# Performance work log

Hardware: AMD Instinct MI355X
Metric: run time of the kernel (lower is better)

The kernel has to match this reference:

```python
import jax, jax.numpy as jnp
import numpy as np

N_NODES = 50000
N_EDGES = 800000
NODE_DIM = 64
EDGE_DIM = 16
HIDDEN = 128
EPS = 1e-5


def _linear_init(key, fan_in, fan_out):
    k1, k2 = jax.random.split(key)
    bound = 1.0 / np.sqrt(fan_in)
    W = jax.random.uniform(k1, (fan_in, fan_out), minval=-bound, maxval=bound, dtype=jnp.float32)
    b = jax.random.uniform(k2, (fan_out,), minval=-bound, maxval=bound, dtype=jnp.float32)
    return W, b


def batchnorm(h, gamma, beta):
    # BatchNorm1d in training mode: batch mean/var (biased), eps=1e-5
    mu = jnp.mean(h, axis=0, keepdims=True)
    var = jnp.mean((h - mu) ** 2, axis=0, keepdims=True)
    return (h - mu) * jax.lax.rsqrt(var + EPS) * gamma + beta


def setup_inputs() -> dict:
    key = jax.random.key(0)
    ks = jax.random.split(key, 8)
    x = jax.random.normal(ks[0], (N_NODES, NODE_DIM), dtype=jnp.float32)
    edge_index = jax.random.randint(ks[1], (2, N_EDGES), 0, N_NODES, dtype=jnp.int64)
    edge_attr = jax.random.normal(ks[2], (N_EDGES, EDGE_DIM), dtype=jnp.float32)
    We1, be1 = _linear_init(ks[3], 2 * NODE_DIM + EDGE_DIM, HIDDEN)
    We2, be2 = _linear_init(ks[4], HIDDEN, HIDDEN)
    Wm, bm = _linear_init(ks[5], HIDDEN, HIDDEN)
    Wn1, bn1 = _linear_init(ks[6], NODE_DIM + HIDDEN, HIDDEN)
    Wn2, bn2 = _linear_init(ks[7], HIDDEN, HIDDEN)
    ones = jnp.ones((HIDDEN,), jnp.float32)
    zeros = jnp.zeros((HIDDEN,), jnp.float32)
    return dict(x=x, edge_index=edge_index, edge_attr=edge_attr,
                We1=We1, be1=be1, ge=ones, bbe=zeros, We2=We2, be2=be2,
                Wm=Wm, bm=bm,
                Wn1=Wn1, bn1=bn1, gn=ones, bbn=zeros, Wn2=Wn2, bn2=bn2)


def reference(x, edge_index, edge_attr, We1, be1, ge, bbe, We2, be2, Wm, bm, Wn1, bn1, gn, bbn, Wn2, bn2):
    row, col = edge_index[0], edge_index[1]
    # gather + concat -> edge network (Linear, BN, ReLU, Linear)
    edge_input = jnp.concatenate([x[row], x[col], edge_attr], axis=-1)  # [E, 2n+e]
    h = jax.nn.relu(batchnorm(edge_input @ We1 + be1, ge, bbe))
    edge_features = h @ We2 + be2
    # message MLP (Linear, ReLU)
    messages = jax.nn.relu(edge_features @ Wm + bm)  # [E, H]
    # scatter-add into source nodes
    agg = jax.ops.segment_sum(messages, row, num_segments=N_NODES)  # [N, H]
    # node network (Linear, BN, ReLU, Linear)
    node_input = jnp.concatenate([x, agg], axis=-1)
    hn = jax.nn.relu(batchnorm(node_input @ Wn1 + bn1, gn, bbn))
    return hn @ Wn2 + bn2
```

## Files before the change

### kernel.cpp

```cpp
#include <hip/hip_runtime.h>
#include <stdint.h>

#define NNODES 50000
#define NEDGES 800000
#define H 128
#define BN_EPS 1e-5f

typedef short short8 __attribute__((ext_vector_type(8)));
typedef float f32x4 __attribute__((ext_vector_type(4)));

__device__ __forceinline__ float bf2f(unsigned short u) {
    unsigned int v = ((unsigned int)u) << 16;
    return __uint_as_float(v);
}
__device__ __forceinline__ unsigned short f2bf(float f) {
    unsigned int x = __float_as_uint(f);
    return (unsigned short)((x + 0x7FFFu + ((x >> 16) & 1u)) >> 16);
}
__device__ __forceinline__ short8 s8z() { short8 z = {0,0,0,0,0,0,0,0}; return z; }

template<int KB>
__device__ __forceinline__ void gemm_tile(const short* __restrict__ sA, const int SK,
                                          const unsigned short* __restrict__ WT, const int RK,
                                          const int n0, f32x4 acc[4][4], const int lane) {
    const int mr = lane & 15, quad = lane >> 4;
    const short* W = (const short*)WT;
    #pragma unroll
    for (int kb = 0; kb < KB; ++kb) {
        short8 a[4];
        #pragma unroll
        for (int mt = 0; mt < 4; ++mt)
            a[mt] = *(const short8*)&sA[(mt*16 + mr)*SK + kb*32 + quad*8];
        #pragma unroll
        for (int nt = 0; nt < 4; ++nt) {
            short8 b = *(const short8*)&W[(size_t)(n0 + nt*16 + mr)*RK + kb*32 + quad*8];
            #pragma unroll
            for (int mt = 0; mt < 4; ++mt)
                acc[mt][nt] = __builtin_amdgcn_mfma_f32_16x16x32_bf16(a[mt], b, acc[mt][nt], 0, 0, 0);
        }
    }
}

__global__ void k_fold(const float* __restrict__ We2, const float* __restrict__ be2,
                       const float* __restrict__ Wm, const float* __restrict__ bm,
                       float* __restrict__ W2m, float* __restrict__ b2m) {
    int j = threadIdx.x;
    int i = blockIdx.x;
    if (i < H) {
        float acc = 0.f;
        for (int k = 0; k < H; ++k) acc = fmaf(We2[i*H + k], Wm[k*H + j], acc);
        W2m[i*H + j] = acc;
    } else {
        float acc = bm[j];
        for (int k = 0; k < H; ++k) acc = fmaf(be2[k], Wm[k*H + j], acc);
        b2m[j] = acc;
    }
}

__global__ void k_prep2(const float* __restrict__ We1, const float* __restrict__ Wn1,
                        const float* __restrict__ Wn2, const float* __restrict__ W2m,
                        unsigned short* __restrict__ WabT, unsigned short* __restrict__ Wn1T,
                        unsigned short* __restrict__ Wn2T, unsigned short* __restrict__ W2mT) {
    int i = blockIdx.x*256 + threadIdx.x;
    if (i < 16384) {
        int n = i >> 6, k = i & 63;
        WabT[n*64 + k] = f2bf(We1[(n < 128 ? k : 64 + k)*H + (n & 127)]);
    } else if (i < 40960) {
        int j = i - 16384; int n = j / 192, k = j - n*192;
        Wn1T[n*192 + k] = f2bf(Wn1[k*H + n]);
    } else if (i < 57344) {
        int j = i - 40960; int n = j >> 7, k = j & 127;
        Wn2T[n*H + k] = f2bf(Wn2[k*H + n]);
    } else if (i < 73728) {
        int j = i - 57344; int n = j >> 7, k = j & 127;
        W2mT[n*H + k] = f2bf(W2m[k*H + n]);
    }
}

__global__ void k_count(const int* __restrict__ ei, int* __restrict__ cnt) {
    int e = blockIdx.x*256 + threadIdx.x;
    if (e < NEDGES) atomicAdd(&cnt[ei[e]], 1);
}

__global__ void k_scan(const int* __restrict__ cnt, int* __restrict__ offsets,
                       int* __restrict__ cursor) {
    __shared__ int wsum[16];
    __shared__ int carry;
    const int tid = threadIdx.x;
    const int lane = tid & 63, wid = tid >> 6;
    if (tid == 0) carry = 0;
    for (int base = 0; base < NNODES; base += 1024) {
        int i = base + tid;
        int v = (i < NNODES) ? cnt[i] : 0;
        int xv = v;
        #pragma unroll
        for (int off = 1; off < 64; off <<= 1) {
            int y = __shfl_up(xv, off);
            if (lane >= off) xv += y;
        }
        if (lane == 63) wsum[wid] = xv;
        __syncthreads();
        if (tid == 0) {
            int a = carry;
            #pragma unroll
            for (int j = 0; j < 16; ++j) { int t = wsum[j]; wsum[j] = a; a += t; }
            carry = a;
        }
        __syncthreads();
        int excl = wsum[wid] + xv - v;
        if (i < NNODES) { offsets[i] = excl; cursor[i] = excl; }
        __syncthreads();
    }
    if (tid == 0) offsets[NNODES] = carry;
}

__global__ void k_scatter(const int* __restrict__ ei, int* __restrict__ cursor,
                          int* __restrict__ elist) {
    int e = blockIdx.x*256 + threadIdx.x;
    if (e < NEDGES) {
        int p = atomicAdd(&cursor[ei[e]], 1);
        elist[p] = e;
    }
}

__launch_bounds__(256)
__global__ void k_T(const float* __restrict__ x, const unsigned short* __restrict__ WabT,
                    unsigned short* __restrict__ T) {
    __shared__ short sA[128*72];
    const int tid = threadIdx.x;
    const int n0b = blockIdx.x*128;
    {
        const int rowl = tid >> 1, half = (tid & 1)*32;
        const int node = n0b + rowl;
        const bool ok = node < NNODES;
        #pragma unroll
        for (int c = 0; c < 4; ++c) {
            int k0 = half + c*8;
            short8 o = s8z();
            if (ok) {
                float4 a = *(const float4*)&x[node*64 + k0];
                float4 b = *(const float4*)&x[node*64 + k0 + 4];
                o[0]=(short)f2bf(a.x); o[1]=(short)f2bf(a.y); o[2]=(short)f2bf(a.z); o[3]=(short)f2bf(a.w);
                o[4]=(short)f2bf(b.x); o[5]=(short)f2bf(b.y); o[6]=(short)f2bf(b.z); o[7]=(short)f2bf(b.w);
            }
            *(short8*)&sA[rowl*72 + k0] = o;
        }
    }
    __syncthreads();
    const int wave = tid >> 6, lane = tid & 63;
    const int m0 = (wave & 1)*64;
    const int n0 = blockIdx.y*128 + (wave >> 1)*64;
    f32x4 acc[4][4];
    f32x4 z = {0.f, 0.f, 0.f, 0.f};
    #pragma unroll
    for (int mt = 0; mt < 4; ++mt)
        #pragma unroll
        for (int nt = 0; nt < 4; ++nt) acc[mt][nt] = z;
    gemm_tile<2>(sA + m0*72, 72, WabT, 64, n0, acc, lane);
    const int mr = lane & 15, quad = lane >> 4;
    #pragma unroll
    for (int nt = 0; nt < 4; ++nt) {
        int j = n0 + nt*16 + mr;
        #pragma unroll
        for (int mt = 0; mt < 4; ++mt) {
            int nb = n0b + m0 + mt*16 + quad*4;
            #pragma unroll
            for (int r = 0; r < 4; ++r) {
                int node = nb + r;
                if (node < NNODES) T[(size_t)node*256 + j] = f2bf(acc[mt][nt][r]);
            }
        }
    }
}

__launch_bounds__(256)
__global__ void k_gather(const unsigned short* __restrict__ T, const int* __restrict__ ei,
                         const float* __restrict__ ea, const float* __restrict__ We1,
                         const float* __restrict__ be1, unsigned short* __restrict__ h1,
                         float* __restrict__ gS, float* __restrict__ gSS) {
    __shared__ float sS[H], sSS[H];
    const int tid = threadIdx.x;
    if (tid < H) { sS[tid] = 0.f; sSS[tid] = 0.f; }
    const int li = tid & 15;
    const int slot = (blockIdx.x*256 + tid) >> 4;
    float4 wcA[16], wcB[16];
    #pragma unroll
    for (int k = 0; k < 16; ++k) {
        wcA[k] = *(const float4*)&We1[(128 + k)*H + li*8];
        wcB[k] = *(const float4*)&We1[(128 + k)*H + li*8 + 4];
    }
    float be[8];
    #pragma unroll
    for (int i = 0; i < 8; ++i) be[i] = be1[li*8 + i];
    float s[8], ss[8];
    #pragma unroll
    for (int i = 0; i < 8; ++i) { s[i] = 0.f; ss[i] = 0.f; }
    for (int it = 0; it < 40; ++it) {
        int e = slot + it*20000;
        int row = ei[e], col = ei[NEDGES + e];
        short8 t1 = *(const short8*)&T[(size_t)row*256 + li*8];
        short8 t2 = *(const short8*)&T[(size_t)col*256 + 128 + li*8];
        float v[8];
        #pragma unroll
        for (int i = 0; i < 8; ++i)
            v[i] = bf2f((unsigned short)t1[i]) + bf2f((unsigned short)t2[i]) + be[i];
        #pragma unroll
        for (int k = 0; k < 16; ++k) {
            float a = ea[e*16 + k];
            v[0] = fmaf(a, wcA[k].x, v[0]); v[1] = fmaf(a, wcA[k].y, v[1]);
            v[2] = fmaf(a, wcA[k].z, v[2]); v[3] = fmaf(a, wcA[k].w, v[3]);
            v[4] = fmaf(a, wcB[k].x, v[4]); v[5] = fmaf(a, wcB[k].y, v[5]);
            v[6] = fmaf(a, wcB[k].z, v[6]); v[7] = fmaf(a, wcB[k].w, v[7]);
        }
        short8 o;
        #pragma unroll
        for (int i = 0; i < 8; ++i) {
            o[i] = (short)f2bf(v[i]);
            s[i] += v[i]; ss[i] += v[i]*v[i];
        }
        *(short8*)&h1[(size_t)e*H + li*8] = o;
    }
    __syncthreads();
    #pragma unroll
    for (int i = 0; i < 8; ++i) {
        atomicAdd(&sS[li*8 + i], s[i]);
        atomicAdd(&sSS[li*8 + i], ss[i]);
    }
    __syncthreads();
    if (tid < H) { atomicAdd(&gS[tid], sS[tid]); atomicAdd(&gSS[tid], sSS[tid]); }
}

__global__ void k_stats(const float* __restrict__ S, const float* __restrict__ SS,
                        const float* __restrict__ g, const float* __restrict__ b,
                        float invCount, float* __restrict__ scale, float* __restrict__ shift) {
    int j = threadIdx.x;
    float mu = S[j]*invCount;
    float var = SS[j]*invCount - mu*mu;
    float sc = rsqrtf(var + BN_EPS)*g[j];
    scale[j] = sc;
    shift[j] = b[j] - mu*sc;
}

__launch_bounds__(256)
__global__ void k_edge2(unsigned short* __restrict__ hb,
                        const float* __restrict__ scale, const float* __restrict__ shift,
                        const unsigned short* __restrict__ W2mT, const float* __restrict__ b2m) {
    __shared__ short sA[128*136];
    const int tid = threadIdx.x;
    const size_t e0 = (size_t)blockIdx.x*128;
    {
        const int rowl = tid >> 1, half = (tid & 1)*64;
        const size_t base = (e0 + rowl)*H + half;
        #pragma unroll
        for (int c = 0; c < 8; ++c) {
            int k0 = half + c*8;
            short8 raw = *(const short8*)&hb[base + c*8];
            float4 sc0 = *(const float4*)&scale[k0], sc1 = *(const float4*)&scale[k0 + 4];
            float4 sh0 = *(const float4*)&shift[k0], sh1 = *(const float4*)&shift[k0 + 4];
            short8 o;
            o[0] = (short)f2bf(fmaxf(fmaf(bf2f((unsigned short)raw[0]), sc0.x, sh0.x), 0.f));
            o[1] = (short)f2bf(fmaxf(fmaf(bf2f((unsigned short)raw[1]), sc0.y, sh0.y), 0.f));
            o[2] = (short)f2bf(fmaxf(fmaf(bf2f((unsigned short)raw[2]), sc0.z, sh0.z), 0.f));
            o[3] = (short)f2bf(fmaxf(fmaf(bf2f((unsigned short)raw[3]), sc0.w, sh0.w), 0.f));
            o[4] = (short)f2bf(fmaxf(fmaf(bf2f((unsigned short)raw[4]), sc1.x, sh1.x), 0.f));
            o[5] = (short)f2bf(fmaxf(fmaf(bf2f((unsigned short)raw[5]), sc1.y, sh1.y), 0.f));
            o[6] = (short)f2bf(fmaxf(fmaf(bf2f((unsigned short)raw[6]), sc1.z, sh1.z), 0.f));
            o[7] = (short)f2bf(fmaxf(fmaf(bf2f((unsigned short)raw[7]), sc1.w, sh1.w), 0.f));
            *(short8*)&sA[rowl*136 + k0] = o;
        }
    }
    __syncthreads();
    const int wave = tid >> 6, lane = tid & 63;
    const int m0 = (wave & 1)*64, n0 = (wave >> 1)*64;
    f32x4 acc[4][4];
    f32x4 z = {0.f, 0.f, 0.f, 0.f};
    #pragma unroll
    for (int mt = 0; mt < 4; ++mt)
        #pragma unroll
        for (int nt = 0; nt < 4; ++nt) acc[mt][nt] = z;
    gemm_tile<4>(sA + m0*136, 136, W2mT, 128, n0, acc, lane);
    const int mr = lane & 15, quad = lane >> 4;
    #pragma unroll
    for (int nt = 0; nt < 4; ++nt) {
        int j = n0 + nt*16 + mr;
        float bias = b2m[j];
        #pragma unroll
        for (int mt = 0; mt < 4; ++mt) {
            size_t eb = e0 + m0 + mt*16 + quad*4;
            #pragma unroll
            for (int r = 0; r < 4; ++r)
                hb[(eb + r)*H + j] = f2bf(fmaxf(acc[mt][nt][r] + bias, 0.f));
        }
    }
}

__launch_bounds__(256)
__global__ void k_agg(const unsigned short* __restrict__ msg, const int* __restrict__ offsets,
                      const int* __restrict__ elist, unsigned short* __restrict__ aggb) {
    const int n = blockIdx.x*4 + (threadIdx.x >> 6);
    const int lane = threadIdx.x & 63;
    const int s0 = offsets[n], t0 = offsets[n + 1];
    float a0 = 0.f, a1 = 0.f;
    for (int i = s0; i < t0; ++i) {
        int e = elist[i];
        unsigned int u = *(const unsigned int*)&msg[(size_t)e*H + lane*2];
        a0 += bf2f((unsigned short)(u & 0xFFFFu));
        a1 += bf2f((unsigned short)(u >> 16));
    }
    unsigned int o = (unsigned int)f2bf(a0) | ((unsigned int)f2bf(a1) << 16);
    *(unsigned int*)&aggb[(size_t)n*H + lane*2] = o;
}

__launch_bounds__(256)
__global__ void k_node1(const float* __restrict__ x, const unsigned short* __restrict__ aggb,
                        const unsigned short* __restrict__ Wn1T, const float* __restrict__ bn1,
                        float* __restrict__ h2, float* __restrict__ gS, float* __restrict__ gSS) {
    __shared__ short sA[128*200];
    __shared__ float sS[H], sSS[H];
    const int tid = threadIdx.x;
    if (tid < H) { sS[tid] = 0.f; sSS[tid] = 0.f; }
    const int n0b = blockIdx.x*128;
    {
        const int rowl = tid >> 1, half = (tid & 1)*96;
        const int node = n0b + rowl;
        const bool ok = node < NNODES;
        #pragma unroll
        for (int c = 0; c < 12; ++c) {
            int k0 = half + c*8;
            short8 o = s8z();
            if (ok) {
                if (k0 < 64) {
                    float4 a = *(const float4*)&x[node*64 + k0];
                    float4 b = *(const float4*)&x[node*64 + k0 + 4];
                    o[0]=(short)f2bf(a.x); o[1]=(short)f2bf(a.y); o[2]=(short)f2bf(a.z); o[3]=(short)f2bf(a.w);
                    o[4]=(short)f2bf(b.x); o[5]=(short)f2bf(b.y); o[6]=(short)f2bf(b.z); o[7]=(short)f2bf(b.w);
                } else {
                    o = *(const short8*)&aggb[(size_t)node*H + (k0 - 64)];
                }
            }
            *(short8*)&sA[rowl*200 + k0] = o;
        }
    }
    __syncthreads();
    const int wave = tid >> 6, lane = tid & 63;
    const int m0 = (wave & 1)*64, n0 = (wave >> 1)*64;
    f32x4 acc[4][4];
    f32x4 z = {0.f, 0.f, 0.f, 0.f};
    #pragma unroll
    for (int mt = 0; mt < 4; ++mt)
        #pragma unroll
        for (int nt = 0; nt < 4; ++nt) acc[mt][nt] = z;
    gemm_tile<6>(sA + m0*200, 200, Wn1T, 192, n0, acc, lane);
    const int mr = lane & 15, quad = lane >> 4;
    #pragma unroll
    for (int nt = 0; nt < 4; ++nt) {
        int j = n0 + nt*16 + mr;
        float bias = bn1[j];
        float s = 0.f, ssum = 0.f;
        #pragma unroll
        for (int mt = 0; mt < 4; ++mt) {
            int nb = n0b + m0 + mt*16 + quad*4;
            #pragma unroll
            for (int r = 0; r < 4; ++r) {
                int node = nb + r;
                if (node < NNODES) {
                    float v = acc[mt][nt][r] + bias;
                    h2[(size_t)node*H + j] = v;
                    s += v; ssum += v*v;
                }
            }
        }
        atomicAdd(&sS[j], s);
        atomicAdd(&sSS[j], ssum);
    }
    __syncthreads();
    if (tid < H) { atomicAdd(&gS[tid], sS[tid]); atomicAdd(&gSS[tid], sSS[tid]); }
}

__launch_bounds__(256)
__global__ void k_node2(const float* __restrict__ h2, const float* __restrict__ scale,
                        const float* __restrict__ shift, const unsigned short* __restrict__ Wn2T,
                        const float* __restrict__ bn2, float* __restrict__ out) {
    __shared__ short sA[128*136];
    const int tid = threadIdx.x;
    const int n0b = blockIdx.x*128;
    {
        const int rowl = tid >> 1, half = (tid & 1)*64;
        const int node = n0b + rowl;
        const bool ok = node < NNODES;
        #pragma unroll
        for (int c = 0; c < 8; ++c) {
            int k0 = half + c*8;
            short8 o = s8z();
            if (ok) {
                float4 a = *(const float4*)&h2[(size_t)node*H + k0];
                float4 b = *(const float4*)&h2[(size_t)node*H + k0 + 4];
                float4 sc0 = *(const float4*)&scale[k0], sc1 = *(const float4*)&scale[k0 + 4];
                float4 sh0 = *(const float4*)&shift[k0], sh1 = *(const float4*)&shift[k0 + 4];
                o[0] = (short)f2bf(fmaxf(fmaf(a.x, sc0.x, sh0.x), 0.f));
                o[1] = (short)f2bf(fmaxf(fmaf(a.y, sc0.y, sh0.y), 0.f));
                o[2] = (short)f2bf(fmaxf(fmaf(a.z, sc0.z, sh0.z), 0.f));
                o[3] = (short)f2bf(fmaxf(fmaf(a.w, sc0.w, sh0.w), 0.f));
                o[4] = (short)f2bf(fmaxf(fmaf(b.x, sc1.x, sh1.x), 0.f));
                o[5] = (short)f2bf(fmaxf(fmaf(b.y, sc1.y, sh1.y), 0.f));
                o[6] = (short)f2bf(fmaxf(fmaf(b.z, sc1.z, sh1.z), 0.f));
                o[7] = (short)f2bf(fmaxf(fmaf(b.w, sc1.w, sh1.w), 0.f));
            }
            *(short8*)&sA[rowl*136 + k0] = o;
        }
    }
    __syncthreads();
    const int wave = tid >> 6, lane = tid & 63;
    const int m0 = (wave & 1)*64, n0 = (wave >> 1)*64;
    f32x4 acc[4][4];
    f32x4 z = {0.f, 0.f, 0.f, 0.f};
    #pragma unroll
    for (int mt = 0; mt < 4; ++mt)
        #pragma unroll
        for (int nt = 0; nt < 4; ++nt) acc[mt][nt] = z;
    gemm_tile<4>(sA + m0*136, 136, Wn2T, 128, n0, acc, lane);
    const int mr = lane & 15, quad = lane >> 4;
    #pragma unroll
    for (int nt = 0; nt < 4; ++nt) {
        int j = n0 + nt*16 + mr;
        float bias = bn2[j];
        #pragma unroll
        for (int mt = 0; mt < 4; ++mt) {
            int nb = n0b + m0 + mt*16 + quad*4;
            #pragma unroll
            for (int r = 0; r < 4; ++r) {
                int node = nb + r;
                if (node < NNODES) out[(size_t)node*H + j] = acc[mt][nt][r] + bias;
            }
        }
    }
}

extern "C" void kernel_launch(void* const* d_in, const int* in_sizes, int n_in,
                              void* d_out, int out_size, void* d_ws, size_t ws_size,
                              hipStream_t stream) {
    (void)in_sizes; (void)n_in; (void)out_size; (void)ws_size;
    const float* x   = (const float*)d_in[0];
    const int*   ei  = (const int*)d_in[1];
    const float* ea  = (const float*)d_in[2];
    const float* We1 = (const float*)d_in[3];
    const float* be1 = (const float*)d_in[4];
    const float* ge  = (const float*)d_in[5];
    const float* bbe = (const float*)d_in[6];
    const float* We2 = (const float*)d_in[7];
    const float* be2 = (const float*)d_in[8];
    const float* Wm  = (const float*)d_in[9];
    const float* bm  = (const float*)d_in[10];
    const float* Wn1 = (const float*)d_in[11];
    const float* bn1 = (const float*)d_in[12];
    const float* gn  = (const float*)d_in[13];
    const float* bbn = (const float*)d_in[14];
    const float* Wn2 = (const float*)d_in[15];
    const float* bn2 = (const float*)d_in[16];
    float* out = (float*)d_out;

    char* ws = (char*)d_ws;
    unsigned short* hb   = (unsigned short*)(ws);
    unsigned short* aggb = (unsigned short*)(ws + 204800000);
    unsigned short* Tbuf = (unsigned short*)(ws + 217600000);
    float*          h2   = (float*)(ws + 217600000);
    int* cnt     = (int*)(ws + 243200000);
    int* offsets = (int*)(ws + 243400000);
    int* cursor  = (int*)(ws + 243600064);
    int* elist   = (int*)(ws + 243800064);
    float* S1     = (float*)(ws + 247000064);
    float* SS1    = S1 + 128;
    float* S2     = S1 + 256;
    float* SS2    = S1 + 384;
    float* scale1 = S1 + 512;
    float* shift1 = S1 + 640;
    float* scale2 = S1 + 768;
    float* shift2 = S1 + 896;
    float* W2m = (float*)(ws + 247004160);
    float* b2m = (float*)(ws + 247069696);
    unsigned short* WabT = (unsigned short*)(ws + 247070208);
    unsigned short* Wn1T = (unsigned short*)(ws + 247102976);
    unsigned short* Wn2T = (unsigned short*)(ws + 247152128);
    unsigned short* W2mT = (unsigned short*)(ws + 247184896);

    hipMemsetAsync(cnt, 0, NNODES*sizeof(int), stream);
    hipMemsetAsync(S1, 0, 512*sizeof(float), stream);

    k_fold<<<H + 1, H, 0, stream>>>(We2, be2, Wm, bm, W2m, b2m);
    k_prep2<<<288, 256, 0, stream>>>(We1, Wn1, Wn2, W2m, WabT, Wn1T, Wn2T, W2mT);
    k_count<<<NEDGES/256, 256, 0, stream>>>(ei, cnt);
    k_scan<<<1, 1024, 0, stream>>>(cnt, offsets, cursor);
    k_scatter<<<NEDGES/256, 256, 0, stream>>>(ei, cursor, elist);
    k_T<<<dim3(391, 2), 256, 0, stream>>>(x, WabT, Tbuf);
    k_gather<<<1250, 256, 0, stream>>>(Tbuf, ei, ea, We1, be1, hb, S1, SS1);
    k_stats<<<1, H, 0, stream>>>(S1, SS1, ge, bbe, 1.0f/NEDGES, scale1, shift1);
    k_edge2<<<NEDGES/128, 256, 0, stream>>>(hb, scale1, shift1, W2mT, b2m);
    k_agg<<<NNODES/4, 256, 0, stream>>>(hb, offsets, elist, aggb);
    k_node1<<<391, 256, 0, stream>>>(x, aggb, Wn1T, bn1, h2, S2, SS2);
    k_stats<<<1, H, 0, stream>>>(S2, SS2, gn, bbn, 1.0f/NNODES, scale2, shift2);
    k_node2<<<391, 256, 0, stream>>>(h2, scale2, shift2, Wn2T, bn2, out);
}
```

Measured before the change: 751.0 us.

## Recompute edge pre-activations in fused edge kernel and segment-reduce messages in-block

The gather kernel now only accumulates BatchNorm statistics and no longer writes the 800k x 128 bf16 pre-activation buffer. A new fused kernel walks edges in CSR (sorted by source) order, recomputes the pre-activation from the projected node table and edge attributes, applies BN and ReLU, runs the folded MLP GEMM, and reduces messages per source node in shared memory. Each run is written directly to an fp32 aggregate buffer, or atomically added when the run spans block boundaries. This removes the large intermediate write and read and the separate aggregation kernel, at the cost of computing the first layer twice, a serial per-column segment scan, and a memset of the aggregate buffer.

```diff
diff --git a/kernel.cpp b/kernel.cpp
--- a/kernel.cpp
+++ b/kernel.cpp
@@ -174,10 +174,10 @@
 }
 
 __launch_bounds__(256)
-__global__ void k_gather(const unsigned short* __restrict__ T, const int* __restrict__ ei,
-                         const float* __restrict__ ea, const float* __restrict__ We1,
-                         const float* __restrict__ be1, unsigned short* __restrict__ h1,
-                         float* __restrict__ gS, float* __restrict__ gSS) {
+__global__ void k_stats_edges(const unsigned short* __restrict__ T, const int* __restrict__ ei,
+                              const float* __restrict__ ea, const float* __restrict__ We1,
+                              const float* __restrict__ be1,
+                              float* __restrict__ gS, float* __restrict__ gSS) {
     __shared__ float sS[H], sSS[H];
     const int tid = threadIdx.x;
     if (tid < H) { sS[tid] = 0.f; sSS[tid] = 0.f; }
@@ -195,30 +195,34 @@
     float s[8], ss[8];
     #pragma unroll
     for (int i = 0; i < 8; ++i) { s[i] = 0.f; ss[i] = 0.f; }
-    for (int it = 0; it < 40; ++it) {
-        int e = slot + it*20000;
+    const float4* ea4 = (const float4*)ea;
+    for (int it = 0; it < 20; ++it) {
+        int e = slot + it*40000;
         int row = ei[e], col = ei[NEDGES + e];
         short8 t1 = *(const short8*)&T[(size_t)row*256 + li*8];
         short8 t2 = *(const short8*)&T[(size_t)col*256 + 128 + li*8];
+        float4 ev[4];
+        #pragma unroll
+        for (int q = 0; q < 4; ++q) ev[q] = ea4[e*4 + q];
         float v[8];
         #pragma unroll
         for (int i = 0; i < 8; ++i)
             v[i] = bf2f((unsigned short)t1[i]) + bf2f((unsigned short)t2[i]) + be[i];
         #pragma unroll
-        for (int k = 0; k < 16; ++k) {
-            float a = ea[e*16 + k];
-            v[0] = fmaf(a, wcA[k].x, v[0]); v[1] = fmaf(a, wcA[k].y, v[1]);
-            v[2] = fmaf(a, wcA[k].z, v[2]); v[3] = fmaf(a, wcA[k].w, v[3]);
-            v[4] = fmaf(a, wcB[k].x, v[4]); v[5] = fmaf(a, wcB[k].y, v[5]);
-            v[6] = fmaf(a, wcB[k].z, v[6]); v[7] = fmaf(a, wcB[k].w, v[7]);
-        }
-        short8 o;
-        #pragma unroll
-        for (int i = 0; i < 8; ++i) {
-            o[i] = (short)f2bf(v[i]);
-            s[i] += v[i]; ss[i] += v[i]*v[i];
-        }
-        *(short8*)&h1[(size_t)e*H + li*8] = o;
+        for (int q = 0; q < 4; ++q) {
+            float aa[4] = {ev[q].x, ev[q].y, ev[q].z, ev[q].w};
+            #pragma unroll
+            for (int kk = 0; kk < 4; ++kk) {
+                int k = q*4 + kk;
+                float a = aa[kk];
+                v[0] = fmaf(a, wcA[k].x, v[0]); v[1] = fmaf(a, wcA[k].y, v[1]);
+                v[2] = fmaf(a, wcA[k].z, v[2]); v[3] = fmaf(a, wcA[k].w, v[3]);
+                v[4] = fmaf(a, wcB[k].x, v[4]); v[5] = fmaf(a, wcB[k].y, v[5]);
+                v[6] = fmaf(a, wcB[k].z, v[6]); v[7] = fmaf(a, wcB[k].w, v[7]);
+            }
+        }
+        #pragma unroll
+        for (int i = 0; i < 8; ++i) { s[i] += v[i]; ss[i] += v[i]*v[i]; }
     }
     __syncthreads();
     #pragma unroll
@@ -242,32 +246,57 @@
 }
 
 __launch_bounds__(256)
-__global__ void k_edge2(unsigned short* __restrict__ hb,
-                        const float* __restrict__ scale, const float* __restrict__ shift,
-                        const unsigned short* __restrict__ W2mT, const float* __restrict__ b2m) {
+__global__ void k_fused(const unsigned short* __restrict__ T, const int* __restrict__ ei,
+                        const int* __restrict__ elist, const int* __restrict__ offsets,
+                        const float* __restrict__ ea, const float* __restrict__ We1,
+                        const float* __restrict__ be1, const float* __restrict__ scale,
+                        const float* __restrict__ shift, const unsigned short* __restrict__ W2mT,
+                        const float* __restrict__ b2m, float* __restrict__ agg) {
     __shared__ short sA[128*136];
+    __shared__ float sWc[16*128];
+    __shared__ int rows[128];
     const int tid = threadIdx.x;
-    const size_t e0 = (size_t)blockIdx.x*128;
-    {
-        const int rowl = tid >> 1, half = (tid & 1)*64;
-        const size_t base = (e0 + rowl)*H + half;
-        #pragma unroll
-        for (int c = 0; c < 8; ++c) {
-            int k0 = half + c*8;
-            short8 raw = *(const short8*)&hb[base + c*8];
-            float4 sc0 = *(const float4*)&scale[k0], sc1 = *(const float4*)&scale[k0 + 4];
-            float4 sh0 = *(const float4*)&shift[k0], sh1 = *(const float4*)&shift[k0 + 4];
-            short8 o;
-            o[0] = (short)f2bf(fmaxf(fmaf(bf2f((unsigned short)raw[0]), sc0.x, sh0.x), 0.f));
-            o[1] = (short)f2bf(fmaxf(fmaf(bf2f((unsigned short)raw[1]), sc0.y, sh0.y), 0.f));
-            o[2] = (short)f2bf(fmaxf(fmaf(bf2f((unsigned short)raw[2]), sc0.z, sh0.z), 0.f));
-            o[3] = (short)f2bf(fmaxf(fmaf(bf2f((unsigned short)raw[3]), sc0.w, sh0.w), 0.f));
-            o[4] = (short)f2bf(fmaxf(fmaf(bf2f((unsigned short)raw[4]), sc1.x, sh1.x), 0.f));
-            o[5] = (short)f2bf(fmaxf(fmaf(bf2f((unsigned short)raw[5]), sc1.y, sh1.y), 0.f));
-            o[6] = (short)f2bf(fmaxf(fmaf(bf2f((unsigned short)raw[6]), sc1.z, sh1.z), 0.f));
-            o[7] = (short)f2bf(fmaxf(fmaf(bf2f((unsigned short)raw[7]), sc1.w, sh1.w), 0.f));
-            *(short8*)&sA[rowl*136 + k0] = o;
-        }
+    const int p0 = blockIdx.x*128;
+    for (int i = tid; i < 2048; i += 256) sWc[i] = We1[16384 + i];
+    const int lp = tid >> 1, half = tid & 1;
+    const int e = elist[p0 + lp];
+    const int row = ei[e], col = ei[NEDGES + e];
+    if (half == 0) rows[lp] = row;
+    const float4* ea4 = (const float4*)ea;
+    float4 ev[4];
+    #pragma unroll
+    for (int q = 0; q < 4; ++q) ev[q] = ea4[e*4 + q];
+    __syncthreads();
+    const int j0 = half*64;
+    #pragma unroll
+    for (int c = 0; c < 8; ++c) {
+        const int jj = j0 + c*8;
+        short8 t1 = *(const short8*)&T[(size_t)row*256 + jj];
+        short8 t2 = *(const short8*)&T[(size_t)col*256 + 128 + jj];
+        float v[8];
+        #pragma unroll
+        for (int i = 0; i < 8; ++i)
+            v[i] = bf2f((unsigned short)t1[i]) + bf2f((unsigned short)t2[i]) + be1[jj + i];
+        #pragma unroll
+        for (int q = 0; q < 4; ++q) {
+            float aa[4] = {ev[q].x, ev[q].y, ev[q].z, ev[q].w};
+            #pragma unroll
+            for (int kk = 0; kk < 4; ++kk) {
+                int k = q*4 + kk;
+                float a = aa[kk];
+                float4 w0 = *(const float4*)&sWc[k*128 + jj];
+                float4 w1 = *(const float4*)&sWc[k*128 + jj + 4];
+                v[0] = fmaf(a, w0.x, v[0]); v[1] = fmaf(a, w0.y, v[1]);
+                v[2] = fmaf(a, w0.z, v[2]); v[3] = fmaf(a, w0.w, v[3]);
+                v[4] = fmaf(a, w1.x, v[4]); v[5] = fmaf(a, w1.y, v[5]);
+                v[6] = fmaf(a, w1.z, v[6]); v[7] = fmaf(a, w1.w, v[7]);
+            }
+        }
+        short8 o;
+        #pragma unroll
+        for (int i = 0; i < 8; ++i)
+            o[i] = (short)f2bf(fmaxf(fmaf(v[i], scale[jj + i], shift[jj + i]), 0.f));
+        *(short8*)&sA[lp*136 + jj] = o;
     }
     __syncthreads();
     const int wave = tid >> 6, lane = tid & 63;
@@ -279,6 +308,7 @@
         #pragma unroll
         for (int nt = 0; nt < 4; ++nt) acc[mt][nt] = z;
     gemm_tile<4>(sA + m0*136, 136, W2mT, 128, n0, acc, lane);
+    __syncthreads();
     const int mr = lane & 15, quad = lane >> 4;
     #pragma unroll
     for (int nt = 0; nt < 4; ++nt) {
@@ -286,33 +316,33 @@
         float bias = b2m[j];
         #pragma unroll
         for (int mt = 0; mt < 4; ++mt) {
-            size_t eb = e0 + m0 + mt*16 + quad*4;
+            int m = m0 + mt*16 + quad*4;
             #pragma unroll
             for (int r = 0; r < 4; ++r)
-                hb[(eb + r)*H + j] = f2bf(fmaxf(acc[mt][nt][r] + bias, 0.f));
+                sA[(m + r)*136 + j] = (short)f2bf(fmaxf(acc[mt][nt][r] + bias, 0.f));
+        }
+    }
+    __syncthreads();
+    if (tid < 128) {
+        const int jf = tid;
+        int p = 0;
+        while (p < 128) {
+            int r = rows[p];
+            int q = p + 1;
+            while (q < 128 && rows[q] == r) ++q;
+            float sum = 0.f;
+            for (int i = p; i < q; ++i) sum += bf2f((unsigned short)sA[i*136 + jf]);
+            bool full = (p0 + p == offsets[r]) && (p0 + q == offsets[r + 1]);
+            float* dst = &agg[(size_t)r*H + jf];
+            if (full) *dst = sum;
+            else atomicAdd(dst, sum);
+            p = q;
         }
     }
 }
 
 __launch_bounds__(256)
-__global__ void k_agg(const unsigned short* __restrict__ msg, const int* __restrict__ offsets,
-                      const int* __restrict__ elist, unsigned short* __restrict__ aggb) {
-    const int n = blockIdx.x*4 + (threadIdx.x >> 6);
-    const int lane = threadIdx.x & 63;
-    const int s0 = offsets[n], t0 = offsets[n + 1];
-    float a0 = 0.f, a1 = 0.f;
-    for (int i = s0; i < t0; ++i) {
-        int e = elist[i];
-        unsigned int u = *(const unsigned int*)&msg[(size_t)e*H + lane*2];
-        a0 += bf2f((unsigned short)(u & 0xFFFFu));
-        a1 += bf2f((unsigned short)(u >> 16));
-    }
-    unsigned int o = (unsigned int)f2bf(a0) | ((unsigned int)f2bf(a1) << 16);
-    *(unsigned int*)&aggb[(size_t)n*H + lane*2] = o;
-}
-
-__launch_bounds__(256)
-__global__ void k_node1(const float* __restrict__ x, const unsigned short* __restrict__ aggb,
+__global__ void k_node1(const float* __restrict__ x, const float* __restrict__ agg,
                         const unsigned short* __restrict__ Wn1T, const float* __restrict__ bn1,
                         float* __restrict__ h2, float* __restrict__ gS, float* __restrict__ gSS) {
     __shared__ short sA[128*200];
@@ -329,14 +359,16 @@
             int k0 = half + c*8;
             short8 o = s8z();
             if (ok) {
+                float4 a, b;
                 if (k0 < 64) {
-                    float4 a = *(const float4*)&x[node*64 + k0];
-                    float4 b = *(const float4*)&x[node*64 + k0 + 4];
-                    o[0]=(short)f2bf(a.x); o[1]=(short)f2bf(a.y); o[2]=(short)f2bf(a.z); o[3]=(short)f2bf(a.w);
-                    o[4]=(short)f2bf(b.x); o[5]=(short)f2bf(b.y); o[6]=(short)f2bf(b.z); o[7]=(short)f2bf(b.w);
+                    a = *(const float4*)&x[node*64 + k0];
+                    b = *(const float4*)&x[node*64 + k0 + 4];
                 } else {
-                    o = *(const short8*)&aggb[(size_t)node*H + (k0 - 64)];
+                    a = *(const float4*)&agg[(size_t)node*H + (k0 - 64)];
+                    b = *(const float4*)&agg[(size_t)node*H + (k0 - 64) + 4];
                 }
+                o[0]=(short)f2bf(a.x); o[1]=(short)f2bf(a.y); o[2]=(short)f2bf(a.z); o[3]=(short)f2bf(a.w);
+                o[4]=(short)f2bf(b.x); o[5]=(short)f2bf(b.y); o[6]=(short)f2bf(b.z); o[7]=(short)f2bf(b.w);
             }
             *(short8*)&sA[rowl*200 + k0] = o;
         }
@@ -460,15 +492,14 @@
     float* out = (float*)d_out;
 
     char* ws = (char*)d_ws;
-    unsigned short* hb   = (unsigned short*)(ws);
-    unsigned short* aggb = (unsigned short*)(ws + 204800000);
-    unsigned short* Tbuf = (unsigned short*)(ws + 217600000);
-    float*          h2   = (float*)(ws + 217600000);
-    int* cnt     = (int*)(ws + 243200000);
-    int* offsets = (int*)(ws + 243400000);
-    int* cursor  = (int*)(ws + 243600064);
-    int* elist   = (int*)(ws + 243800064);
-    float* S1     = (float*)(ws + 247000064);
+    unsigned short* Tbuf = (unsigned short*)(ws);
+    float* agg = (float*)(ws + 25600000);
+    float* h2  = (float*)(ws + 51200000);
+    int* cnt     = (int*)(ws + 76800000);
+    int* offsets = (int*)(ws + 77000192);
+    int* cursor  = (int*)(ws + 77200256);
+    int* elist   = (int*)(ws + 77400320);
+    float* S1     = (float*)(ws + 80600384);
     float* SS1    = S1 + 128;
     float* S2     = S1 + 256;
     float* SS2    = S1 + 384;
@@ -476,15 +507,16 @@
     float* shift1 = S1 + 640;
     float* scale2 = S1 + 768;
     float* shift2 = S1 + 896;
-    float* W2m = (float*)(ws + 247004160);
-    float* b2m = (float*)(ws + 247069696);
-    unsigned short* WabT = (unsigned short*)(ws + 247070208);
-    unsigned short* Wn1T = (unsigned short*)(ws + 247102976);
-    unsigned short* Wn2T = (unsigned short*)(ws + 247152128);
-    unsigned short* W2mT = (unsigned short*)(ws + 247184896);
+    float* W2m = (float*)(ws + 80604480);
+    float* b2m = (float*)(ws + 80670016);
+    unsigned short* WabT = (unsigned short*)(ws + 80670592);
+    unsigned short* Wn1T = (unsigned short*)(ws + 80703360);
+    unsigned short* Wn2T = (unsigned short*)(ws + 80752512);
+    unsigned short* W2mT = (unsigned short*)(ws + 80785280);
 
     hipMemsetAsync(cnt, 0, NNODES*sizeof(int), stream);
     hipMemsetAsync(S1, 0, 512*sizeof(float), stream);
+    hipMemsetAsync(agg, 0, (size_t)NNODES*H*sizeof(float), stream);
 
     k_fold<<<H + 1, H, 0, stream>>>(We2, be2, Wm, bm, W2m, b2m);
     k_prep2<<<288, 256, 0, stream>>>(We1, Wn1, Wn2, W2m, WabT, Wn1T, Wn2T, W2mT);
@@ -492,11 +524,11 @@
     k_scan<<<1, 1024, 0, stream>>>(cnt, offsets, cursor);
     k_scatter<<<NEDGES/256, 256, 0, stream>>>(ei, cursor, elist);
     k_T<<<dim3(391, 2), 256, 0, stream>>>(x, WabT, Tbuf);
-    k_gather<<<1250, 256, 0, stream>>>(Tbuf, ei, ea, We1, be1, hb, S1, SS1);
+    k_stats_edges<<<2500, 256, 0, stream>>>(Tbuf, ei, ea, We1, be1, S1, SS1);
     k_stats<<<1, H, 0, stream>>>(S1, SS1, ge, bbe, 1.0f/NEDGES, scale1, shift1);
-    k_edge2<<<NEDGES/128, 256, 0, stream>>>(hb, scale1, shift1, W2mT, b2m);
-    k_agg<<<NNODES/4, 256, 0, stream>>>(hb, offsets, elist, aggb);
-    k_node1<<<391, 256, 0, stream>>>(x, aggb, Wn1T, bn1, h2, S2, SS2);
+    k_fused<<<NEDGES/128, 256, 0, stream>>>(Tbuf, ei, elist, offsets, ea, We1, be1,
+                                            scale1, shift1, W2mT, b2m, agg);
+    k_node1<<<391, 256, 0, stream>>>(x, agg, Wn1T, bn1, h2, S2, SS2);
     k_stats<<<1, H, 0, stream>>>(S2, SS2, gn, bbn, 1.0f/NNODES, scale2, shift2);
     k_node2<<<391, 256, 0, stream>>>(h2, scale2, shift2, Wn2T, bn2, out);
 }
```

Result: slower. 885.1 us (+17.9%).

## Process edges in sorted-by-source order and use MFMA for edge-attr projection

Applied to the files above, without the earlier changes.

The gather kernel now walks edges in CSR (sorted-by-row) order via elist and writes hidden activations at sorted positions. This lets the aggregation kernel read messages contiguously without the elist indirection. The 16-wide edge-attribute projection moves from per-thread scalar FMAs with register-held weights to a bf16 MFMA tile against a new transposed, zero-padded weight matrix. The changes trade extra shared-memory staging and bf16 rounding of edge_attr and of the T sum for coalesced aggregation reads and lower register pressure.

```diff
diff --git a/kernel.cpp b/kernel.cpp
--- a/kernel.cpp
+++ b/kernel.cpp
@@ -60,7 +60,8 @@
 __global__ void k_prep2(const float* __restrict__ We1, const float* __restrict__ Wn1,
                         const float* __restrict__ Wn2, const float* __restrict__ W2m,
                         unsigned short* __restrict__ WabT, unsigned short* __restrict__ Wn1T,
-                        unsigned short* __restrict__ Wn2T, unsigned short* __restrict__ W2mT) {
+                        unsigned short* __restrict__ Wn2T, unsigned short* __restrict__ W2mT,
+                        unsigned short* __restrict__ WcT) {
     int i = blockIdx.x*256 + threadIdx.x;
     if (i < 16384) {
         int n = i >> 6, k = i & 63;
@@ -74,6 +75,9 @@
     } else if (i < 73728) {
         int j = i - 57344; int n = j >> 7, k = j & 127;
         W2mT[n*H + k] = f2bf(W2m[k*H + n]);
+    } else if (i < 77824) {
+        int j = i - 73728; int n = j >> 5, k = j & 31;
+        WcT[n*32 + k] = (k < 16) ? f2bf(We1[(128 + k)*H + n]) : (unsigned short)0;
     }
 }
 
@@ -174,57 +178,71 @@
 }
 
 __launch_bounds__(256)
-__global__ void k_gather(const unsigned short* __restrict__ T, const int* __restrict__ ei,
-                         const float* __restrict__ ea, const float* __restrict__ We1,
-                         const float* __restrict__ be1, unsigned short* __restrict__ h1,
-                         float* __restrict__ gS, float* __restrict__ gSS) {
+__global__ void k_gather2(const unsigned short* __restrict__ T, const int* __restrict__ ei,
+                          const int* __restrict__ elist, const float* __restrict__ ea,
+                          const unsigned short* __restrict__ WcT, const float* __restrict__ be1,
+                          unsigned short* __restrict__ hb,
+                          float* __restrict__ gS, float* __restrict__ gSS) {
+    __shared__ short sEa[128*40];
+    __shared__ short sT[128*136];
     __shared__ float sS[H], sSS[H];
     const int tid = threadIdx.x;
     if (tid < H) { sS[tid] = 0.f; sSS[tid] = 0.f; }
-    const int li = tid & 15;
-    const int slot = (blockIdx.x*256 + tid) >> 4;
-    float4 wcA[16], wcB[16];
-    #pragma unroll
-    for (int k = 0; k < 16; ++k) {
-        wcA[k] = *(const float4*)&We1[(128 + k)*H + li*8];
-        wcB[k] = *(const float4*)&We1[(128 + k)*H + li*8 + 4];
-    }
-    float be[8];
-    #pragma unroll
-    for (int i = 0; i < 8; ++i) be[i] = be1[li*8 + i];
-    float s[8], ss[8];
-    #pragma unroll
-    for (int i = 0; i < 8; ++i) { s[i] = 0.f; ss[i] = 0.f; }
-    for (int it = 0; it < 40; ++it) {
-        int e = slot + it*20000;
-        int row = ei[e], col = ei[NEDGES + e];
-        short8 t1 = *(const short8*)&T[(size_t)row*256 + li*8];
-        short8 t2 = *(const short8*)&T[(size_t)col*256 + 128 + li*8];
-        float v[8];
-        #pragma unroll
-        for (int i = 0; i < 8; ++i)
-            v[i] = bf2f((unsigned short)t1[i]) + bf2f((unsigned short)t2[i]) + be[i];
-        #pragma unroll
-        for (int k = 0; k < 16; ++k) {
-            float a = ea[e*16 + k];
-            v[0] = fmaf(a, wcA[k].x, v[0]); v[1] = fmaf(a, wcA[k].y, v[1]);
-            v[2] = fmaf(a, wcA[k].z, v[2]); v[3] = fmaf(a, wcA[k].w, v[3]);
-            v[4] = fmaf(a, wcB[k].x, v[4]); v[5] = fmaf(a, wcB[k].y, v[5]);
-            v[6] = fmaf(a, wcB[k].z, v[6]); v[7] = fmaf(a, wcB[k].w, v[7]);
-        }
+    const int p0 = blockIdx.x*128;
+    const int lp = tid >> 1, half = tid & 1;
+    const int e = elist[p0 + lp];
+    const int row = ei[e], col = ei[NEDGES + e];
+    {
+        const float4* ea4 = (const float4*)ea;
+        float4 a = ea4[e*4 + half*2];
+        float4 b = ea4[e*4 + half*2 + 1];
         short8 o;
-        #pragma unroll
-        for (int i = 0; i < 8; ++i) {
-            o[i] = (short)f2bf(v[i]);
-            s[i] += v[i]; ss[i] += v[i]*v[i];
-        }
-        *(short8*)&h1[(size_t)e*H + li*8] = o;
-    }
-    __syncthreads();
-    #pragma unroll
-    for (int i = 0; i < 8; ++i) {
-        atomicAdd(&sS[li*8 + i], s[i]);
-        atomicAdd(&sSS[li*8 + i], ss[i]);
+        o[0]=(short)f2bf(a.x); o[1]=(short)f2bf(a.y); o[2]=(short)f2bf(a.z); o[3]=(short)f2bf(a.w);
+        o[4]=(short)f2bf(b.x); o[5]=(short)f2bf(b.y); o[6]=(short)f2bf(b.z); o[7]=(short)f2bf(b.w);
+        *(short8*)&sEa[lp*40 + half*8] = o;
+        *(short8*)&sEa[lp*40 + 16 + half*8] = s8z();
+    }
+    {
+        #pragma unroll
+        for (int c = 0; c < 8; ++c) {
+            int jj = half*64 + c*8;
+            short8 t1 = *(const short8*)&T[(size_t)row*256 + jj];
+            short8 t2 = *(const short8*)&T[(size_t)col*256 + 128 + jj];
+            short8 o;
+            #pragma unroll
+            for (int i = 0; i < 8; ++i)
+                o[i] = (short)f2bf(bf2f((unsigned short)t1[i]) + bf2f((unsigned short)t2[i]));
+            *(short8*)&sT[lp*136 + jj] = o;
+        }
+    }
+    __syncthreads();
+    const int wave = tid >> 6, lane = tid & 63;
+    const int m0 = (wave & 1)*64, n0 = (wave >> 1)*64;
+    f32x4 acc[4][4];
+    f32x4 z = {0.f, 0.f, 0.f, 0.f};
+    #pragma unroll
+    for (int mt = 0; mt < 4; ++mt)
+        #pragma unroll
+        for (int nt = 0; nt < 4; ++nt) acc[mt][nt] = z;
+    gemm_tile<1>(sEa + m0*40, 40, WcT, 32, n0, acc, lane);
+    const int mr = lane & 15, quad = lane >> 4;
+    #pragma unroll
+    for (int nt = 0; nt < 4; ++nt) {
+        int j = n0 + nt*16 + mr;
+        float bia = be1[j];
+        float s = 0.f, ssum = 0.f;
+        #pragma unroll
+        for (int mt = 0; mt < 4; ++mt) {
+            int m = m0 + mt*16 + quad*4;
+            #pragma unroll
+            for (int r = 0; r < 4; ++r) {
+                float v = acc[mt][nt][r] + bf2f((unsigned short)sT[(m + r)*136 + j]) + bia;
+                hb[(size_t)(p0 + m + r)*H + j] = f2bf(v);
+                s += v; ssum += v*v;
+            }
+        }
+        atomicAdd(&sS[j], s);
+        atomicAdd(&sSS[j], ssum);
     }
     __syncthreads();
     if (tid < H) { atomicAdd(&gS[tid], sS[tid]); atomicAdd(&gSS[tid], sSS[tid]); }
@@ -296,14 +314,13 @@
 
 __launch_bounds__(256)
 __global__ void k_agg(const unsigned short* __restrict__ msg, const int* __restrict__ offsets,
-                      const int* __restrict__ elist, unsigned short* __restrict__ aggb) {
+                      unsigned short* __restrict__ aggb) {
     const int n = blockIdx.x*4 + (threadIdx.x >> 6);
     const int lane = threadIdx.x & 63;
     const int s0 = offsets[n], t0 = offsets[n + 1];
     float a0 = 0.f, a1 = 0.f;
-    for (int i = s0; i < t0; ++i) {
-        int e = elist[i];
-        unsigned int u = *(const unsigned int*)&msg[(size_t)e*H + lane*2];
+    for (int p = s0; p < t0; ++p) {
+        unsigned int u = *(const unsigned int*)&msg[(size_t)p*H + lane*2];
         a0 += bf2f((unsigned short)(u & 0xFFFFu));
         a1 += bf2f((unsigned short)(u >> 16));
     }
@@ -465,10 +482,10 @@
     unsigned short* Tbuf = (unsigned short*)(ws + 217600000);
     float*          h2   = (float*)(ws + 217600000);
     int* cnt     = (int*)(ws + 243200000);
-    int* offsets = (int*)(ws + 243400000);
-    int* cursor  = (int*)(ws + 243600064);
-    int* elist   = (int*)(ws + 243800064);
-    float* S1     = (float*)(ws + 247000064);
+    int* offsets = (int*)(ws + 243400192);
+    int* cursor  = (int*)(ws + 243600256);
+    int* elist   = (int*)(ws + 243800320);
+    float* S1     = (float*)(ws + 247000384);
     float* SS1    = S1 + 128;
     float* S2     = S1 + 256;
     float* SS2    = S1 + 384;
@@ -476,26 +493,27 @@
     float* shift1 = S1 + 640;
     float* scale2 = S1 + 768;
     float* shift2 = S1 + 896;
-    float* W2m = (float*)(ws + 247004160);
-    float* b2m = (float*)(ws + 247069696);
-    unsigned short* WabT = (unsigned short*)(ws + 247070208);
-    unsigned short* Wn1T = (unsigned short*)(ws + 247102976);
-    unsigned short* Wn2T = (unsigned short*)(ws + 247152128);
-    unsigned short* W2mT = (unsigned short*)(ws + 247184896);
+    float* W2m = (float*)(ws + 247004480);
+    float* b2m = (float*)(ws + 247070016);
+    unsigned short* WabT = (unsigned short*)(ws + 247070592);
+    unsigned short* Wn1T = (unsigned short*)(ws + 247103360);
+    unsigned short* Wn2T = (unsigned short*)(ws + 247152512);
+    unsigned short* W2mT = (unsigned short*)(ws + 247185280);
+    unsigned short* WcT  = (unsigned short*)(ws + 247218048);
 
     hipMemsetAsync(cnt, 0, NNODES*sizeof(int), stream);
     hipMemsetAsync(S1, 0, 512*sizeof(float), stream);
 
     k_fold<<<H + 1, H, 0, stream>>>(We2, be2, Wm, bm, W2m, b2m);
-    k_prep2<<<288, 256, 0, stream>>>(We1, Wn1, Wn2, W2m, WabT, Wn1T, Wn2T, W2mT);
+    k_prep2<<<304, 256, 0, stream>>>(We1, Wn1, Wn2, W2m, WabT, Wn1T, Wn2T, W2mT, WcT);
     k_count<<<NEDGES/256, 256, 0, stream>>>(ei, cnt);
     k_scan<<<1, 1024, 0, stream>>>(cnt, offsets, cursor);
     k_scatter<<<NEDGES/256, 256, 0, stream>>>(ei, cursor, elist);
     k_T<<<dim3(391, 2), 256, 0, stream>>>(x, WabT, Tbuf);
-    k_gather<<<1250, 256, 0, stream>>>(Tbuf, ei, ea, We1, be1, hb, S1, SS1);
+    k_gather2<<<NEDGES/128, 256, 0, stream>>>(Tbuf, ei, elist, ea, WcT, be1, hb, S1, SS1);
     k_stats<<<1, H, 0, stream>>>(S1, SS1, ge, bbe, 1.0f/NEDGES, scale1, shift1);
     k_edge2<<<NEDGES/128, 256, 0, stream>>>(hb, scale1, shift1, W2mT, b2m);
-    k_agg<<<NNODES/4, 256, 0, stream>>>(hb, offsets, elist, aggb);
+    k_agg<<<NNODES/4, 256, 0, stream>>>(hb, offsets, aggb);
     k_node1<<<391, 256, 0, stream>>>(x, aggb, Wn1T, bn1, h2, S2, SS2);
     k_stats<<<1, H, 0, stream>>>(S2, SS2, gn, bbn, 1.0f/NNODES, scale2, shift2);
     k_node2<<<391, 256, 0, stream>>>(h2, scale2, shift2, Wn2T, bn2, out);
```

New measurement: 733.3 us. -2.3%, faster.
